# Optimization experiments

Measured on AMD Instinct MI355X. Metric: run time of the kernel, lower is better.

The kernel has to match this reference:

```python
import jax, jax.numpy as jnp
import numpy as np

M1 = M2 = M3 = 6  # retained Fourier modes per axis (matches init_kwargs)
TWO_PI = 2.0 * np.pi


def _freq_grid(kx, ky, kz):
    KX, KY, KZ = jnp.meshgrid(kx, ky, kz, indexing='ij')
    return jnp.stack([KX.ravel(), KY.ravel(), KZ.ravel()], axis=-1)  # [M, 3]


def _cplx(w):
    return w[..., 0] + 1j * w[..., 1]


def setup_inputs() -> dict:
    key = jax.random.key(0)
    k1, k2, k3, k4, k5, k6 = jax.random.split(key, 6)
    B, C, N = 2, 32, 8192
    scale = 1.0 / (C * C)
    return {
        'x': jax.random.normal(k1, (B, C, N), dtype=jnp.float32),
        'pos': jax.random.uniform(k2, (B, N, 3), dtype=jnp.float32),
        'w1': scale * jax.random.uniform(k3, (C, C, M1, M2, M3, 2), dtype=jnp.float32),
        'w2': scale * jax.random.uniform(k4, (C, C, M1, M2, M3, 2), dtype=jnp.float32),
        'w3': scale * jax.random.uniform(k5, (C, C, M1, M2, M3, 2), dtype=jnp.float32),
        'w4': scale * jax.random.uniform(k6, (C, C, M1, M2, M3, 2), dtype=jnp.float32),
    }


def reference(x, pos, w1, w2, w3, w4):
    m1, m2, m3 = M1, M2, M3
    B, C, N = x.shape
    # FFT-ordered frequencies: [0..m-1, -m..-1]
    kx = jnp.concatenate([jnp.arange(m1), jnp.arange(-m1, 0)]).astype(jnp.float32)
    ky = jnp.concatenate([jnp.arange(m2), jnp.arange(-m2, 0)]).astype(jnp.float32)
    kz_full = jnp.concatenate([jnp.arange(m3), jnp.arange(-m3, 0)]).astype(jnp.float32)
    kz_half = jnp.arange(m3).astype(jnp.float32)
    Kf = _freq_grid(kx, ky, kz_full)                     # [M, 3], M = 2m1*2m2*2m3
    Kh = _freq_grid(kx, ky, kz_half)                     # [Mh, 3], Mh = 2m1*2m2*m3
    Ki = jnp.concatenate([Kh, -Kh[::-1]], axis=0)        # [2Mh, 3] Hermitian extension

    # Nonuniform forward Fourier transform (transformer.forward), fused with permutes:
    V_fwd = jnp.exp(-1j * TWO_PI * jnp.einsum('md,bnd->bmn', Kf, pos))  # [B, M, N]
    x_ft = jnp.einsum('bmn,bcn->bcm', V_fwd, x.astype(jnp.complex64))   # [B, C, M]
    x_ft = x_ft.reshape(B, C, 2 * m1, 2 * m2, 2 * m3)

    def mul(a, w):
        return jnp.einsum('bixyz,ioxyz->boxyz', a, _cplx(w))

    out = jnp.zeros((B, C, 2 * m1, 2 * m2, m3), dtype=jnp.complex64)
    out = out.at[:, :, :m1, :m2, :].set(mul(x_ft[:, :, :m1, :m2, :m3], w1))
    out = out.at[:, :, m1:, :m2, :].set(mul(x_ft[:, :, m1:, :m2, :m3], w2))
    out = out.at[:, :, :m1, m2:, :].set(mul(x_ft[:, :, :m1, m2:, :m3], w3))
    out = out.at[:, :, m1:, m2:, :].set(mul(x_ft[:, :, m1:, m2:, :m3], w4))

    xf = out.reshape(B, C, -1)                           # [B, C, Mh]
    xf2 = jnp.conj(xf[:, ::-1, ::-1])                    # torch flip(-1,-2).conj()
    xf = jnp.concatenate([xf, xf2], axis=-1)             # [B, C, 2Mh]

    # Nonuniform inverse transform (transformer.inverse), fused with permutes:
    V_inv = jnp.exp(1j * TWO_PI * jnp.einsum('kd,bnd->bnk', Ki, pos))   # [B, N, 2Mh]
    y = jnp.einsum('bnk,bck->bcn', V_inv, xf)            # [B, C, N]
    return (y / N * 2.0).real.astype(jnp.float32)
```

## Files before the change

### kernel.cpp

```cpp
#include <hip/hip_runtime.h>

#define TWOPI 6.28318530717958647692f

#define BB 2
#define CC 32
#define NN 8192

typedef short bf16x8 __attribute__((ext_vector_type(8)));
typedef float f32x4  __attribute__((ext_vector_type(4)));

__device__ __forceinline__ float2 cmul(float2 a, float2 b){
    return make_float2(fmaf(a.x, b.x, -(a.y*b.y)), fmaf(a.x, b.y, a.y*b.x));
}
__device__ __forceinline__ float2 conj2(float2 a){ return make_float2(a.x, -a.y); }
__device__ __forceinline__ unsigned pk_bf16(float lo, float hi){
    unsigned r;
    asm("v_cvt_pk_bf16_f32 %0, %1, %2" : "=v"(r) : "v"(lo), "v"(hi));
    return r;
}
__device__ __forceinline__ float hw_sin(float p){
    float r; asm("v_sin_f32 %0, %1" : "=v"(r) : "v"(p)); return r;
}
__device__ __forceinline__ float hw_cos(float p){
    float r; asm("v_cos_f32 %0, %1" : "=v"(r) : "v"(p)); return r;
}
__device__ __forceinline__ short f2bf(float x){
    union { float f; unsigned u; } v; v.f = x;
    unsigned r = v.u + (0x7fffu + ((v.u >> 16) & 1u));
    return (short)(r >> 16);
}

__global__ __launch_bounds__(256)
void wtrans_kernel(const float* __restrict__ w1, const float* __restrict__ w2,
                   const float* __restrict__ w3, const float* __restrict__ w4,
                   float* __restrict__ wt){
    const int abz = blockIdx.x;
    const int q   = blockIdx.y;
    const float* w = (q==0)?w1:(q==1)?w2:(q==2)?w3:w4;
    const int tid = threadIdx.x;
    #pragma unroll
    for (int k=0;k<4;k++){
        int iop = tid + k*256;
        float2 v = *(const float2*)(w + ((size_t)iop*216 + abz)*2);
        *(float2*)(wt + (((size_t)q*216 + abz)*1024 + iop)*2) = v;
    }
}

__global__ __launch_bounds__(256, 4)
void fused_fwd_kernel(const float* __restrict__ x, const float* __restrict__ pos,
                      const float* __restrict__ w1, const float* __restrict__ w2,
                      const float* __restrict__ w3, const float* __restrict__ w4,
                      float* __restrict__ wt, float* __restrict__ part){
    __shared__ short  P2[12][16][72];
    __shared__ short  xl[32][72];

    const int bid = blockIdx.x;
    const int tid = threadIdx.x;

    if (bid >= 576){
        const int wid = bid - 576;
        const int abz = wid % 216;
        const int q   = wid / 216;
        const float* w = (q==0)?w1:(q==1)?w2:(q==2)?w3:w4;
        #pragma unroll
        for (int k=0;k<4;k++){
            int iop = tid + k*256;
            float2 v = *(const float2*)(w + ((size_t)iop*216 + abz)*2);
            *(float2*)(wt + (((size_t)q*216 + abz)*1024 + iop)*2) = v;
        }
        return;
    }

    const int ks  = bid & 31;
    const int bm  = (bid >> 5) % 9;
    const int b   = bid / 288;
    const int l   = tid & 63;
    const int w   = tid >> 6;
    const int cid = 4*bm + w;
    const int c4k = cid / 9;
    const int lc  = cid % 9;
    const int kxb = (c4k==0) ? 0 : (c4k==1) ? 3 : (c4k==2) ? -6 : -3;
    const int kx0 = kxb + lc/3;
    const int lm3 = lc % 3;

    f32x4 acc[3][2];
    #pragma unroll
    for (int i=0;i<3;i++)
      #pragma unroll
      for (int j=0;j<2;j++) acc[i][j] = (f32x4){0.f,0.f,0.f,0.f};

    #pragma unroll 1
    for (int rnd=0; rnd<4; ++rnd){
        const int n0 = ks*256 + rnd*64;
        __syncthreads();
        #pragma unroll
        for (int k=0;k<2;k++){
            int idx = k*256 + tid;
            int c = idx >> 4;
            int j = idx & 15;
            float4 v = *(const float4*)(x + ((size_t)b*CC + c)*NN + n0 + j*4);
            unsigned p0 = pk_bf16(v.x, v.y);
            unsigned p1 = pk_bf16(v.z, v.w);
            *(uint2*)(&xl[c][j*4]) = make_uint2(p0, p1);
        }
        {
            const int n = n0 + l;
            const float px = pos[((size_t)b*NN + n)*3 + 0];
            const float py = pos[((size_t)b*NN + n)*3 + 1];
            const float pz = pos[((size_t)b*NN + n)*3 + 2];
            const float2 Exf = make_float2(hw_cos(px), -hw_sin(px));
            const float2 Eyf = make_float2(hw_cos(py), -hw_sin(py));
            const float2 Ezf = make_float2(hw_cos(pz), -hw_sin(pz));
            float2 e = make_float2(1.f, 0.f);
            const int ax = kx0 < 0 ? -kx0 : kx0;
            #pragma unroll
            for (int i2=0;i2<6;i2++) if (i2 < ax) e = cmul(e, Exf);
            if (kx0 < 0) e = conj2(e);
            const float2 y2  = cmul(Eyf, Eyf);
            const float2 y4  = cmul(y2, y2);
            if      (lm3 == 1) e = cmul(e, y4);
            else if (lm3 == 2) e = cmul(e, conj2(y4));
            const float2 y8  = cmul(y4, y4);
            const float2 y11 = cmul(cmul(y8, y2), Eyf);
            float2 Sv[4];
            Sv[0] = e;
            Sv[1] = cmul(Sv[0], Eyf);
            Sv[2] = cmul(Sv[1], (lm3==1) ? conj2(y11) : Eyf);
            Sv[3] = cmul(Sv[2], Eyf);
            #pragma unroll
            for (int s2=0; s2<4; ++s2){
                float2 ee = Sv[s2];
                #pragma unroll
                for (int kz=0; kz<6; ++kz){
                    const int g  = 6*s2 + kz;
                    const int g3 = g >> 3;
                    const int j  = g & 7;
                    unsigned pv = pk_bf16(ee.x, ee.y);
                    P2[w*3+g3][2*j  ][l] = (short)(pv & 0xffffu);
                    P2[w*3+g3][2*j+1][l] = (short)(pv >> 16);
                    if (kz < 5) ee = cmul(ee, Ezf);
                }
            }
        }
        __syncthreads();
        #pragma unroll
        for (int kstep=0; kstep<2; ++kstep){
            const int kn = kstep*32 + (l>>4)*8;
            bf16x8 bfr0 = *(const bf16x8*)(&xl[(l&15)     ][kn]);
            bf16x8 bfr1 = *(const bf16x8*)(&xl[(l&15) + 16][kn]);
            #pragma unroll
            for (int g3=0; g3<3; ++g3){
                bf16x8 afr = *(const bf16x8*)(&P2[w*3+g3][l&15][kn]);
                acc[g3][0] = __builtin_amdgcn_mfma_f32_16x16x32_bf16(afr, bfr0, acc[g3][0],0,0,0);
                acc[g3][1] = __builtin_amdgcn_mfma_f32_16x16x32_bf16(afr, bfr1, acc[g3][1],0,0,0);
            }
        }
    }
    const int Rb = cid*48;
    #pragma unroll
    for (int g3=0; g3<3; ++g3)
      #pragma unroll
      for (int nt=0; nt<2; ++nt)
        #pragma unroll
        for (int r=0; r<4; ++r){
            const int R = Rb + g3*16 + (l>>4)*4 + r;
            const int C = (l&15) + nt*16;
            part[(((size_t)ks*BB + b)*1728 + R)*32 + C] = acc[g3][nt][r];
        }
}

__global__ __launch_bounds__(128, 2)
void fwd_atomic_kernel(const float* __restrict__ x, const float* __restrict__ pos,
                       float* __restrict__ F){
    const int tid = threadIdx.x;
    const int colslot = tid & 15;
    const int cs = tid >> 4;
    const int col = blockIdx.y * 16 + colslot;
    const int ixm = col / 12;
    const int iym = col % 12;
    const int b   = blockIdx.z;
    const int nb0 = blockIdx.x * 128;

    __shared__ float2 exl[12][65];
    __shared__ float2 eyl[12][65];
    __shared__ float2 ezt[64][8];
    __shared__ float  xl[CC][68];

    float acc[6][4][2];
    #pragma unroll
    for (int z=0;z<6;z++)
      #pragma unroll
      for (int j=0;j<4;j++){ acc[z][j][0]=0.f; acc[z][j][1]=0.f; }

    for (int t=0; t<2; ++t){
        const int nb = nb0 + t*64;
        __syncthreads();
        if (tid < 64){
            const int n = nb + tid;
            const float px = pos[((size_t)b*NN + n)*3 + 0];
            const float py = pos[((size_t)b*NN + n)*3 + 1];
            const float pz = pos[((size_t)b*NN + n)*3 + 2];
            float s, c;
            float2 pw[7];
            s = hw_sin(px); c = hw_cos(px);
            { float2 e1 = make_float2(c, -s);
              pw[0] = make_float2(1.f, 0.f);
              #pragma unroll
              for (int k=1;k<7;k++) pw[k] = cmul(pw[k-1], e1);
              #pragma unroll
              for (int k=0;k<6;k++) exl[k][tid] = pw[k];
              #pragma unroll
              for (int k=6;k<12;k++) exl[k][tid] = make_float2(pw[12-k].x, -pw[12-k].y);
            }
            s = hw_sin(py); c = hw_cos(py);
            { float2 e1 = make_float2(c, -s);
              pw[0] = make_float2(1.f, 0.f);
              #pragma unroll
              for (int k=1;k<7;k++) pw[k] = cmul(pw[k-1], e1);
              #pragma unroll
              for (int k=0;k<6;k++) eyl[k][tid] = pw[k];
              #pragma unroll
              for (int k=6;k<12;k++) eyl[k][tid] = make_float2(pw[12-k].x, -pw[12-k].y);
            }
            s = hw_sin(pz); c = hw_cos(pz);
            { float2 e1 = make_float2(c, -s);
              float2 qv = make_float2(1.f, 0.f);
              #pragma unroll
              for (int k=0;k<6;k++){ ezt[tid][k] = qv; qv = cmul(qv, e1); }
            }
        }
        #pragma unroll
        for (int k=0;k<4;k++){
            int v = tid + k*128;
            int c = v >> 4;
            int j = v & 15;
            float4 xv = *(const float4*)(x + (size_t)(b*CC + c)*NN + nb + j*4);
            *(float4*)(&xl[c][j*4]) = xv;
        }
        __syncthreads();

        #pragma unroll 2
        for (int np=0; np<64; ++np){
            float2 rex = exl[ixm][np];
            float2 rey = eyl[iym][np];
            float2 exy = cmul(rex, rey);
            float xv0 = xl[cs*4+0][np];
            float xv1 = xl[cs*4+1][np];
            float xv2 = xl[cs*4+2][np];
            float xv3 = xl[cs*4+3][np];
            const float4* ezp = (const float4*)(&ezt[np][0]);
            float4 ea = ezp[0], eb2 = ezp[1], ec = ezp[2];
            float2 ezv[6];
            ezv[0] = make_float2(ea.x, ea.y);  ezv[1] = make_float2(ea.z, ea.w);
            ezv[2] = make_float2(eb2.x, eb2.y); ezv[3] = make_float2(eb2.z, eb2.w);
            ezv[4] = make_float2(ec.x, ec.y);  ezv[5] = make_float2(ec.z, ec.w);
            #pragma unroll
            for (int z=0; z<6; ++z){
                float2 ph = cmul(exy, ezv[z]);
                acc[z][0][0] = fmaf(ph.x, xv0, acc[z][0][0]);
                acc[z][0][1] = fmaf(ph.y, xv0, acc[z][0][1]);
                acc[z][1][0] = fmaf(ph.x, xv1, acc[z][1][0]);
                acc[z][1][1] = fmaf(ph.y, xv1, acc[z][1][1]);
                acc[z][2][0] = fmaf(ph.x, xv2, acc[z][2][0]);
                acc[z][2][1] = fmaf(ph.y, xv2, acc[z][2][1]);
                acc[z][3][0] = fmaf(ph.x, xv3, acc[z][3][0]);
                acc[z][3][1] = fmaf(ph.y, xv3, acc[z][3][1]);
            }
        }
    }

    const int c0 = cs*4;
    const int c4f = ixm/3;
    const int tb  = (ixm%3)*72 + iym*6;
    #pragma unroll
    for (int z=0;z<6;z++)
      #pragma unroll
      for (int j=0;j<4;j++){
        const int R = c4f*432 + 2*(tb + z);
        float* p = F + ((size_t)b*1728 + R)*32 + c0 + j;
        atomicAdd(p,      acc[z][j][0]);
        atomicAdd(p + 32, acc[z][j][1]);
      }
}

template<int NK>
__global__ __launch_bounds__(128)
void mix_kernel(const float* __restrict__ part, const float* __restrict__ wt,
                short* __restrict__ Abf){
    const int tid = threadIdx.x;
    const int o  = tid & 31;
    const int ml = tid >> 5;
    const int b  = blockIdx.y;
    const int m0 = blockIdx.x * 4;

    __shared__ float xs[256];
    __shared__ float os[4][32][2];

    const int r0 = (m0/216)*432 + 2*(m0%216);
    {
        const float* pb = part + (((size_t)b*1728 + r0)*32) + 2*tid;
        float s0 = 0.f, s1 = 0.f;
        #pragma unroll 8
        for (int k=0;k<NK;k++){
            float2 v = *(const float2*)(pb + (size_t)k*110592);
            s0 += v.x; s1 += v.y;
        }
        xs[2*tid]   = s0;
        xs[2*tid+1] = s1;
    }
    __syncthreads();

    const int m  = m0 + ml;
    const int ix = m / 72;
    const int iy = (m / 6) % 12;
    const int iz = m % 6;
    const int q  = (ix>=6 ? 1 : 0) + (iy>=6 ? 2 : 0);
    const int a  = ix % 6;
    const int bb2 = iy % 6;
    const int abz = (a*6 + bb2)*6 + iz;
    const float* wq = wt + ((size_t)q*216 + abz)*2048;

    float orr = 0.f, oii = 0.f;
    #pragma unroll 8
    for (int i=0;i<32;i++){
        float xr = xs[ml*64 + i];
        float xi = xs[ml*64 + 32 + i];
        float2 wv = *(const float2*)(wq + (i*32 + o)*2);
        orr = fmaf(xr, wv.x, orr); orr = fmaf(-xi, wv.y, orr);
        oii = fmaf(xr, wv.y, oii); oii = fmaf( xi, wv.x, oii);
    }
    os[ml][o][0] = orr;
    os[ml][o][1] = oii;
    __syncthreads();
    if (o < 16){
        const float sc2 = 2.0f / (float)NN;
        float tr =  (os[ml][o][0] + os[ml][31-o][0]) * sc2;
        float ti = -((os[ml][o][1] + os[ml][31-o][1]) * sc2);
        const int mc4 = m / 216;
        const int mr  = m % 216;
        const int kk  = mr >> 2;
        const int qq  = mr & 3;
        unsigned pv = pk_bf16(tr, ti);
        *(unsigned*)(Abf + (size_t)b*27648 + (((size_t)o*54 + kk)*4 + mc4)*8 + 2*qq) = pv;
    }
}

__global__ __launch_bounds__(768)
void inv_kernel(const float* __restrict__ pos, const short* __restrict__ Abf,
                float* __restrict__ y){
    const int tid = threadIdx.x;
    const int og  = tid >> 8;
    const int w4  = (tid >> 6) & 3;
    const int l   = tid & 63;
    const int col = l & 15;
    const int c4  = l >> 4;
    const int b   = blockIdx.y;
    const int n   = blockIdx.x*64 + w4*16 + col;

    __shared__ float red[2][4][16][17];

    const float px = pos[((size_t)b*NN + n)*3 + 0];
    const float py = pos[((size_t)b*NN + n)*3 + 1];
    const float pz = pos[((size_t)b*NN + n)*3 + 2];
    const float2 Ex = make_float2(hw_cos(px), hw_sin(px));
    const float2 Ey = make_float2(hw_cos(py), hw_sin(py));
    const float2 Ez = make_float2(hw_cos(pz), hw_sin(pz));

    const float2 yy2 = cmul(Ey, Ey);
    const float2 yy4 = cmul(yy2, yy2);
    const float2 yy8 = cmul(yy4, yy4);
    const float2 cj11 = conj2(cmul(cmul(yy8, yy2), Ey));
    const float2 x3  = cmul(cmul(Ex, Ex), Ex);
    const float2 x6  = cmul(x3, x3);
    float2 e = (c4==0) ? make_float2(1.f, 0.f)
             : (c4==1) ? x3
             : (c4==2) ? conj2(x6)
             :           conj2(x3);
    if (og >= 1) e = cmul(e, Ex);
    if (og == 2) e = cmul(e, Ex);

    const short* Ab = Abf + (size_t)b*27648 + (((size_t)col*54)*4 + (size_t)c4)*8
                          + (size_t)og*18*32;
    f32x4 acc = {0.f, 0.f, 0.f, 0.f};

    union BU { unsigned u[4]; bf16x8 v; };

    float2 S  = e;
    float2 ee = S;
    #pragma unroll
    for (int u2=0; u2<18; ++u2){
        BU bu;
        #pragma unroll
        for (int qq=0; qq<4; ++qq){
            const int g = 4*u2 + qq;
            if (g > 0){
                if (g % 6) ee = cmul(ee, Ez);
                else { S = cmul(S, (g==36) ? cj11 : Ey); ee = S; }
            }
            bu.u[qq] = pk_bf16(ee.x, ee.y);
        }
        bf16x8 afr = *(const bf16x8*)(Ab + (size_t)u2*32);
        acc = __builtin_amdgcn_mfma_f32_16x16x32_bf16(afr, bu.v, acc, 0, 0, 0);
    }

    if (og >= 1){
        #pragma unroll
        for (int r=0; r<4; ++r) red[og-1][w4][c4*4 + r][col] = acc[r];
    }
    __syncthreads();
    if (og == 0){
        float* yb = y + (size_t)b*CC*NN + n;
        #pragma unroll
        for (int r=0; r<4; ++r){
            const int ch = c4*4 + r;
            float v = acc[r] + red[0][w4][ch][col] + red[1][w4][ch][col];
            yb[(size_t)ch*NN]      = v;
            yb[(size_t)(31-ch)*NN] = v;
        }
    }
}

extern "C" void kernel_launch(void* const* d_in, const int* in_sizes, int n_in,
                              void* d_out, int out_size, void* d_ws, size_t ws_size,
                              hipStream_t stream){
    const float* x   = (const float*)d_in[0];
    const float* pos = (const float*)d_in[1];
    const float* w1  = (const float*)d_in[2];
    const float* w2  = (const float*)d_in[3];
    const float* w3  = (const float*)d_in[4];
    const float* w4  = (const float*)d_in[5];
    float* out = (float*)d_out;
    char* wsb = (char*)d_ws;

    float* wt    = (float*)(wsb);
    short* Abf   = (short*)(wsb + 7520256);
    float* part2 = (float*)(wsb + 7741440);
    const bool use_part = (ws_size >= 21897216ull);

    if (use_part){
        fused_fwd_kernel<<<dim3(1440), 256, 0, stream>>>(x, pos, w1, w2, w3, w4, wt, part2);
        mix_kernel<32><<<dim3(216,2), 128, 0, stream>>>(part2, wt, Abf);
    } else {
        wtrans_kernel<<<dim3(216,4), 256, 0, stream>>>(w1, w2, w3, w4, wt);
        hipMemsetAsync(part2, 0, 442368, stream);
        fwd_atomic_kernel<<<dim3(64,9,2), 128, 0, stream>>>(x, pos, part2);
        mix_kernel<1><<<dim3(216,2), 128, 0, stream>>>(part2, wt, Abf);
    }

    inv_kernel<<<dim3(NN/64, BB), 768, 0, stream>>>(pos, Abf, out);
}
```

Measured before the change: 36.03 us.

## Store partial sums and inverse operand in MFMA fragment-native layout

The forward partial-sum buffer now uses a fragment-ordered layout, so each lane writes its MFMA accumulator as one 16-byte vector store instead of scattered scalar stores. The atomic forward path writes into the same layout through a new index helper, and the mix kernel decodes it back when reducing. The bf16 operand buffer for the inverse kernel is reordered so a wavefront's A-fragment loads are contiguous per lane. The change targets uncoalesced stores and loads, at the cost of more complex index arithmetic in the mix kernel and in the atomics.

After: 32.22 us. 1.12x faster.

```diff
diff --git a/kernel.cpp b/kernel.cpp
--- a/kernel.cpp
+++ b/kernel.cpp
@@ -24,10 +24,11 @@
 __device__ __forceinline__ float hw_cos(float p){
     float r; asm("v_cos_f32 %0, %1" : "=v"(r) : "v"(p)); return r;
 }
-__device__ __forceinline__ short f2bf(float x){
-    union { float f; unsigned u; } v; v.f = x;
-    unsigned r = v.u + (0x7fffu + ((v.u >> 16) & 1u));
-    return (short)(r >> 16);
+
+__device__ __forceinline__ size_t fragoff(int R, int C){
+    int cid = R/48, g3 = (R%48)/16, frow = R%16;
+    int nt = C>>4, ll = (frow>>2)*16 + (C&15), r = frow&3;
+    return ((size_t)cid*3 + g3)*512 + (size_t)nt*256 + (size_t)ll*4 + r;
 }
 
 __global__ __launch_bounds__(256)
@@ -156,17 +157,12 @@
             }
         }
     }
-    const int Rb = cid*48;
+    float* pb = part + ((((size_t)ks*BB + b)*36 + cid)*3)*512;
     #pragma unroll
     for (int g3=0; g3<3; ++g3)
       #pragma unroll
       for (int nt=0; nt<2; ++nt)
-        #pragma unroll
-        for (int r=0; r<4; ++r){
-            const int R = Rb + g3*16 + (l>>4)*4 + r;
-            const int C = (l&15) + nt*16;
-            part[(((size_t)ks*BB + b)*1728 + R)*32 + C] = acc[g3][nt][r];
-        }
+        *(f32x4*)(pb + (size_t)(g3*2+nt)*256 + (size_t)l*4) = acc[g3][nt];
 }
 
 __global__ __launch_bounds__(128, 2)
@@ -272,14 +268,14 @@
     const int c0 = cs*4;
     const int c4f = ixm/3;
     const int tb  = (ixm%3)*72 + iym*6;
+    float* Fb = F + (size_t)b*55296;
     #pragma unroll
     for (int z=0;z<6;z++)
       #pragma unroll
       for (int j=0;j<4;j++){
         const int R = c4f*432 + 2*(tb + z);
-        float* p = F + ((size_t)b*1728 + R)*32 + c0 + j;
-        atomicAdd(p,      acc[z][j][0]);
-        atomicAdd(p + 32, acc[z][j][1]);
+        atomicAdd(Fb + fragoff(R,   c0 + j), acc[z][j][0]);
+        atomicAdd(Fb + fragoff(R+1, c0 + j), acc[z][j][1]);
       }
 }
 
@@ -296,17 +292,29 @@
     __shared__ float xs[256];
     __shared__ float os[4][32][2];
 
-    const int r0 = (m0/216)*432 + 2*(m0%216);
     {
-        const float* pb = part + (((size_t)b*1728 + r0)*32) + 2*tid;
+        const int mm0 = m0 % 216, c4m = m0 / 216;
+        const int q0  = 2*mm0;
+        const int cid = c4m*9 + q0/48;
+        const int g3  = (q0 % 48) / 16;
+        const int lh  = (q0 % 16) >> 3;
+        const int v   = 2*tid;
+        const int nt  = v >> 7;
+        const int rem = v & 127;
+        const int lp  = rem >> 2;
+        const int rr  = rem & 3;
+        const float* pb = part + (((size_t)b*36 + cid)*3 + g3)*512
+                        + (size_t)nt*256 + (size_t)(lh*32 + lp)*4 + rr;
         float s0 = 0.f, s1 = 0.f;
         #pragma unroll 8
         for (int k=0;k<NK;k++){
-            float2 v = *(const float2*)(pb + (size_t)k*110592);
-            s0 += v.x; s1 += v.y;
-        }
-        xs[2*tid]   = s0;
-        xs[2*tid+1] = s1;
+            float2 vv = *(const float2*)(pb + (size_t)k*110592);
+            s0 += vv.x; s1 += vv.y;
+        }
+        const int jA = ((lp>>4)<<2) + rr;
+        const int ci = nt*16 + (lp & 15);
+        xs[jA*32 + ci]       = s0;
+        xs[(jA+1)*32 + ci]   = s1;
     }
     __syncthreads();
 
@@ -341,7 +349,7 @@
         const int kk  = mr >> 2;
         const int qq  = mr & 3;
         unsigned pv = pk_bf16(tr, ti);
-        *(unsigned*)(Abf + (size_t)b*27648 + (((size_t)o*54 + kk)*4 + mc4)*8 + 2*qq) = pv;
+        *(unsigned*)(Abf + (size_t)b*27648 + ((size_t)kk*64 + mc4*16 + o)*8 + 2*qq) = pv;
     }
 }
 
@@ -379,8 +387,7 @@
     if (og >= 1) e = cmul(e, Ex);
     if (og == 2) e = cmul(e, Ex);
 
-    const short* Ab = Abf + (size_t)b*27648 + (((size_t)col*54)*4 + (size_t)c4)*8
-                          + (size_t)og*18*32;
+    const short* Ab = Abf + (size_t)b*27648 + (size_t)og*18*512 + (size_t)l*8;
     f32x4 acc = {0.f, 0.f, 0.f, 0.f};
 
     union BU { unsigned u[4]; bf16x8 v; };
@@ -399,7 +406,7 @@
             }
             bu.u[qq] = pk_bf16(ee.x, ee.y);
         }
-        bf16x8 afr = *(const bf16x8*)(Ab + (size_t)u2*32);
+        bf16x8 afr = *(const bf16x8*)(Ab + (size_t)u2*512);
         acc = __builtin_amdgcn_mfma_f32_16x16x32_bf16(afr, bu.v, acc, 0, 0, 0);
     }
 
```
